# Performance work log

Hardware: AMD Instinct MI355X
Metric: run time of the kernel (lower is better)

The kernel has to match this reference:

```python
import jax, jax.numpy as jnp
import numpy as np

B, C, E, TOPK = 8192, 1024, 8, 4
H = 4 * C  # mlp_ratio = 4.0
EPS = 1e-6


def quick_gelu(x):
    return x * jax.nn.sigmoid(1.702 * x)


def layer_norm(x, gamma, beta):
    mu = jnp.mean(x, axis=-1, keepdims=True)
    var = jnp.var(x, axis=-1, keepdims=True)
    return (x - mu) * jax.lax.rsqrt(var + EPS) * gamma + beta


def setup_inputs() -> dict:
    key = jax.random.key(0)
    ks = jax.random.split(key, 8)
    s1 = 1.0 / np.sqrt(C)
    s2 = 1.0 / np.sqrt(H)
    return {
        "x": jax.random.normal(ks[0], (B, C), dtype=jnp.float32),
        "W1": jax.random.uniform(ks[1], (E, C, H), jnp.float32, -s1, s1),
        "b1": jax.random.uniform(ks[2], (E, H), jnp.float32, -s1, s1),
        "W2": jax.random.uniform(ks[3], (E, H, C), jnp.float32, -s2, s2),
        "b2": jax.random.uniform(ks[4], (E, C), jnp.float32, -s2, s2),
        "ln_g": jnp.ones((E, C), jnp.float32),
        "ln_b": jnp.zeros((E, C), jnp.float32),
        "Wg": jax.random.uniform(ks[5], (C, E), jnp.float32, -s1, s1),
        "bg": jax.random.uniform(ks[6], (E,), jnp.float32, -s1, s1),
    }


def reference(x, W1, b1, W2, b2, ln_g, ln_b, Wg, bg):
    # gate + softmax + top-k
    scores = jax.nn.softmax(x @ Wg + bg, axis=-1)           # [B, E]
    topk_scores, topk_idx = jax.lax.top_k(scores, TOPK)     # [B, K]
    # all experts on all tokens (naive MoE, matches original)
    h = quick_gelu(jnp.einsum('bc,ech->beh', x, W1) + b1)   # [B, E, H]
    y = quick_gelu(jnp.einsum('beh,ehc->bec', h, W2) + b2)  # [B, E, C]
    y = layer_norm(y, ln_g, ln_b)                            # [B, E, C]
    # gather top-k expert outputs and weighted-combine
    topk_out = jnp.take_along_axis(y, topk_idx[:, :, None], axis=1)  # [B, K, C]
    return jnp.sum(topk_out * topk_scores[:, :, None], axis=1)       # [B, C]
```

## Files before the change

### kernel.cpp

```cpp
#include <hip/hip_runtime.h>

#define NB 8192
#define NC 1024
#define NE 8
#define NK 4
#define NH 4096
constexpr int ROWCAP = NB * NK + NE * 128;

typedef _Float16 f16;
typedef _Float16 f16x8 __attribute__((ext_vector_type(8)));
typedef _Float16 f16x4 __attribute__((ext_vector_type(4)));
typedef float    f32x4 __attribute__((ext_vector_type(4)));

__device__ __forceinline__ void async_cp16(const f16* g, f16* l) {
    __builtin_amdgcn_global_load_lds((const __attribute__((address_space(1))) void*)g,
                                     (__attribute__((address_space(3))) void*)l, 16, 0, 0);
}

__device__ __forceinline__ float quick_gelu(float v) {
    return v / (1.f + __expf(-1.702f * v));
}

__global__ void transpose_cast_k(const float* __restrict__ in, f16* __restrict__ out,
                                 int R, int S) {
    __shared__ f16 tile[32][33];
    int e = blockIdx.z;
    long base = (long)e * R * S;
    int s0 = blockIdx.x * 32, r0 = blockIdx.y * 32;
    int tx = threadIdx.x & 31, ty = threadIdx.x >> 5;
    #pragma unroll
    for (int i = 0; i < 32; i += 8)
        tile[ty + i][tx] = (f16)in[base + (long)(r0 + ty + i) * S + s0 + tx];
    __syncthreads();
    #pragma unroll
    for (int i = 0; i < 32; i += 8)
        out[base + (long)(s0 + ty + i) * R + r0 + tx] = tile[tx][ty + i];
}

__global__ void gating_k(const float* __restrict__ x, const float* __restrict__ Wg,
                         const float* __restrict__ bg, int* __restrict__ counts,
                         int* __restrict__ tokmap, int* __restrict__ eids,
                         int* __restrict__ slots, float* __restrict__ gatew,
                         f16* __restrict__ x16) {
    int b = blockIdx.x, t = threadIdx.x;
    float acc[NE] = {};
    float4 xv = ((const float4*)(x + (long)b * NC))[t];
    f16x4 hx = { (f16)xv.x, (f16)xv.y, (f16)xv.z, (f16)xv.w };
    ((f16x4*)(x16 + (long)b * NC))[t] = hx;
    const float* wr = Wg + (long)t * 4 * NE;
    #pragma unroll
    for (int j = 0; j < 4; j++) {
        float xj = ((const float*)&xv)[j];
        #pragma unroll
        for (int e2 = 0; e2 < NE; e2++) acc[e2] += xj * wr[j * NE + e2];
    }
    #pragma unroll
    for (int e2 = 0; e2 < NE; e2++)
        #pragma unroll
        for (int off = 32; off; off >>= 1) acc[e2] += __shfl_down(acc[e2], off);
    __shared__ float red[4][NE];
    int lane = t & 63, w = t >> 6;
    if (lane == 0)
        for (int e2 = 0; e2 < NE; e2++) red[w][e2] = acc[e2];
    __syncthreads();
    if (t == 0) {
        float l[NE];
        float m = -1e30f;
        for (int e2 = 0; e2 < NE; e2++) {
            l[e2] = red[0][e2] + red[1][e2] + red[2][e2] + red[3][e2] + bg[e2];
            m = fmaxf(m, l[e2]);
        }
        float p[NE], sum = 0.f;
        for (int e2 = 0; e2 < NE; e2++) { p[e2] = __expf(l[e2] - m); sum += p[e2]; }
        float inv = 1.f / sum;
        for (int e2 = 0; e2 < NE; e2++) p[e2] *= inv;
        bool taken[NE] = {};
        for (int k = 0; k < NK; k++) {
            int be = 0; float bv = -1e30f;
            for (int e2 = 0; e2 < NE; e2++)
                if (!taken[e2] && p[e2] > bv) { bv = p[e2]; be = e2; }
            taken[be] = true;
            int slot = atomicAdd(&counts[be], 1);
            tokmap[be * NB + slot] = b;
            eids[b * NK + k] = be;
            slots[b * NK + k] = slot;
            gatew[b * NK + k] = bv;
        }
    }
}

__global__ void offsets_k(const int* __restrict__ counts, int* __restrict__ offp) {
    if (threadIdx.x == 0 && blockIdx.x == 0) {
        int o = 0;
        for (int e = 0; e < NE; e++) { offp[e] = o; o += ((counts[e] + 127) >> 7) << 7; }
    }
}

__global__ __launch_bounds__(256) void gemm_f16(
    const f16* __restrict__ A, const f16* __restrict__ Bt,
    const float* __restrict__ bias, f16* __restrict__ Out,
    const int* __restrict__ counts, const int* __restrict__ offp,
    const int* __restrict__ tokmap, int Kd, int N, int gather) {
    int e = blockIdx.z;
    int cnt = counts[e];
    int m0 = blockIdx.x << 7;
    if (m0 >= cnt) return;
    int n0 = blockIdx.y << 7;
    int base = offp[e];

    __shared__ __align__(16) f16 smem[16384];

    int t = threadIdx.x;
    int lane = t & 63;
    int w = t >> 6;
    int wm = (w >> 1) << 6, wn = (w & 1) << 6;

    int sr = m0 + (t >> 2);
    int sc = (((t & 3) ^ ((t >> 3) & 3)) << 3);
    int ca = sr < cnt - 1 ? sr : cnt - 1;
    int cb = sr + 64 < cnt - 1 ? sr + 64 : cnt - 1;
    long arow0, arow1;
    if (gather) { arow0 = tokmap[e * NB + ca]; arow1 = tokmap[e * NB + cb]; }
    else        { arow0 = base + ca;           arow1 = base + cb; }
    const f16* ap0 = A + arow0 * (long)Kd + sc;
    const f16* ap1 = A + arow1 * (long)Kd + sc;
    const f16* bp0 = Bt + ((long)e * N + n0 + (t >> 2)) * (long)Kd + sc;
    const f16* bp1 = bp0 + (long)64 * Kd;

    auto stage = [&](int q) {
        f16* d = smem + (q << 13) + (t << 3);
        async_cp16(ap0, d);        ap0 += 32;
        async_cp16(ap1, d + 2048); ap1 += 32;
        async_cp16(bp0, d + 4096); bp0 += 32;
        async_cp16(bp1, d + 6144); bp1 += 32;
    };

    f32x4 acc[4][4] = {};
    int ml = lane & 15;
    int sxq = (((lane >> 4) ^ ((ml >> 1) & 3)) << 3);
    int aoff = (wm + ml) * 32 + sxq;
    int boff = (wn + ml) * 32 + sxq + 4096;

    int nIter = Kd >> 5;
    stage(0);
    __syncthreads();
    for (int it = 0; it < nIter; ++it) {
        int p = it & 1;
        if (it + 1 < nIter) stage(p ^ 1);
        const f16* sb = smem + (p << 13);
        f16x8 af[4], bf[4];
        #pragma unroll
        for (int mi = 0; mi < 4; mi++) af[mi] = *(const f16x8*)(sb + aoff + mi * 512);
        #pragma unroll
        for (int ni = 0; ni < 4; ni++) bf[ni] = *(const f16x8*)(sb + boff + ni * 512);
        #pragma unroll
        for (int mi = 0; mi < 4; mi++)
            #pragma unroll
            for (int ni = 0; ni < 4; ni++)
                acc[mi][ni] = __builtin_amdgcn_mfma_f32_16x16x32_f16(af[mi], bf[ni], acc[mi][ni], 0, 0, 0);
        __syncthreads();
    }

    const int EP = 136;
    int rq = (lane >> 4) << 2;
    #pragma unroll
    for (int h = 0; h < 2; ++h) {
        if (wm == h * 64) {
            #pragma unroll
            for (int ni = 0; ni < 4; ni++) {
                int col = wn + ni * 16 + ml;
                float bv = bias[(long)e * N + n0 + col];
                #pragma unroll
                for (int mi = 0; mi < 4; mi++) {
                    #pragma unroll
                    for (int rr = 0; rr < 4; rr++) {
                        int lr = mi * 16 + rq + rr;
                        smem[lr * EP + col] = (f16)quick_gelu(acc[mi][ni][rr] + bv);
                    }
                }
            }
        }
        __syncthreads();
        int r = t >> 2;
        int grow = m0 + h * 64 + r;
        if (grow < cnt) {
            long gbase = (long)(base + grow) * N + n0;
            #pragma unroll
            for (int j = 0; j < 4; j++) {
                int cc = ((t & 3) + 4 * j) << 3;
                *(f16x8*)(Out + gbase + cc) = *(const f16x8*)&smem[r * EP + cc];
            }
        }
        __syncthreads();
    }
}

__global__ void ln_combine_k(const f16* __restrict__ y16, const float* __restrict__ lng,
                             const float* __restrict__ lnb, const int* __restrict__ eids,
                             const int* __restrict__ slots, const float* __restrict__ gatew,
                             const int* __restrict__ offp, float* __restrict__ out) {
    int b = blockIdx.x, t = threadIdx.x;
    int lane = t & 63, w = t >> 6;
    __shared__ float red[4][2];
    float o[4] = {0.f, 0.f, 0.f, 0.f};
    int c0 = t * 4;
    for (int k = 0; k < NK; k++) {
        int e = eids[b * NK + k];
        long r = offp[e] + slots[b * NK + k];
        float wk = gatew[b * NK + k];
        f16x4 hv = *(const f16x4*)(y16 + r * NC + c0);
        float v[4];
        #pragma unroll
        for (int j = 0; j < 4; j++) v[j] = (float)hv[j];
        float s = v[0] + v[1] + v[2] + v[3];
        float ss = v[0] * v[0] + v[1] * v[1] + v[2] * v[2] + v[3] * v[3];
        #pragma unroll
        for (int off = 32; off; off >>= 1) { s += __shfl_down(s, off); ss += __shfl_down(ss, off); }
        if (lane == 0) { red[w][0] = s; red[w][1] = ss; }
        __syncthreads();
        float S  = red[0][0] + red[1][0] + red[2][0] + red[3][0];
        float SS = red[0][1] + red[1][1] + red[2][1] + red[3][1];
        float mu = S * (1.f / NC);
        float var = SS * (1.f / NC) - mu * mu;
        float rs = rsqrtf(var + 1e-6f);
        #pragma unroll
        for (int j = 0; j < 4; j++) {
            float g  = lng[(long)e * NC + c0 + j];
            float bb = lnb[(long)e * NC + c0 + j];
            o[j] += wk * ((v[j] - mu) * rs * g + bb);
        }
        __syncthreads();
    }
    float4 ov = {o[0], o[1], o[2], o[3]};
    ((float4*)(out + (long)b * NC))[t] = ov;
}

extern "C" void kernel_launch(void* const* d_in, const int* in_sizes, int n_in,
                              void* d_out, int out_size, void* d_ws, size_t ws_size,
                              hipStream_t stream) {
    const float* x   = (const float*)d_in[0];
    const float* W1  = (const float*)d_in[1];
    const float* b1  = (const float*)d_in[2];
    const float* W2  = (const float*)d_in[3];
    const float* b2  = (const float*)d_in[4];
    const float* lng = (const float*)d_in[5];
    const float* lnb = (const float*)d_in[6];
    const float* Wg  = (const float*)d_in[7];
    const float* bg  = (const float*)d_in[8];
    float* out = (float*)d_out;

    char* ws = (char*)d_ws;
    size_t o = 0;
    auto take = [&](size_t bytes) { char* p = ws + o; o += (bytes + 255) & ~(size_t)255; return p; };
    f16*   x16    = (f16*)take((size_t)NB * NC * 2);
    f16*   w1t    = (f16*)take((size_t)NE * NH * NC * 2);
    f16*   w2t    = (f16*)take((size_t)NE * NC * NH * 2);
    f16*   h16    = (f16*)take((size_t)ROWCAP * NH * 2);
    f16*   y16    = (f16*)take((size_t)ROWCAP * NC * 2);
    int*   tokmap = (int*)take((size_t)NE * NB * 4);
    int*   eids   = (int*)take((size_t)NB * NK * 4);
    int*   slots  = (int*)take((size_t)NB * NK * 4);
    float* gatew  = (float*)take((size_t)NB * NK * 4);
    int*   counts = (int*)take(256);
    int*   offp   = (int*)take(256);

    hipMemsetAsync(counts, 0, NE * sizeof(int), stream);
    transpose_cast_k<<<dim3(NH / 32, NC / 32, NE), 256, 0, stream>>>(W1, w1t, NC, NH);
    transpose_cast_k<<<dim3(NC / 32, NH / 32, NE), 256, 0, stream>>>(W2, w2t, NH, NC);
    gating_k<<<NB, 256, 0, stream>>>(x, Wg, bg, counts, tokmap, eids, slots, gatew, x16);
    offsets_k<<<1, 64, 0, stream>>>(counts, offp);
    gemm_f16<<<dim3(64, NH / 128, NE), 256, 0, stream>>>(x16, w1t, b1, h16, counts, offp, tokmap, NC, NH, 1);
    gemm_f16<<<dim3(64, NC / 128, NE), 256, 0, stream>>>(h16, w2t, b2, y16, counts, offp, tokmap, NH, NC, 0);
    ln_combine_k<<<NB, 256, 0, stream>>>(y16, lng, lnb, eids, slots, gatew, offp, out);
}
```

Measured before the change: 1.859 ms.

## Replace expert GEMM with 256x256 tile, 4-stage async pipeline, split waits

Replaces the 128x128, 256-thread, double-buffered expert GEMM with a 256x256 tile run by 512 threads. It adds a four-slab LDS ring with async global-to-LDS copies three slabs ahead, explicit vmcnt/lgkmcnt waits and barriers, and raised wave priority around the MFMA bursts. Each wave computes its M half in two passes so loads of the next A fragments overlap the current MFMAs. The aim is more reuse per LDS byte and more overlap of loads with compute. The trade-offs are that the XOR swizzle on LDS is dropped, which may cause bank conflicts, the 128 KB LDS footprint limits occupancy, and 256-row tiles waste more work on partially filled expert segments.

```diff
diff --git a/kernel.cpp b/kernel.cpp
--- a/kernel.cpp
+++ b/kernel.cpp
@@ -96,99 +96,130 @@
     }
 }
 
-__global__ __launch_bounds__(256) void gemm_f16(
+__global__ __launch_bounds__(512, 2) void gemm256(
     const f16* __restrict__ A, const f16* __restrict__ Bt,
     const float* __restrict__ bias, f16* __restrict__ Out,
     const int* __restrict__ counts, const int* __restrict__ offp,
     const int* __restrict__ tokmap, int Kd, int N, int gather) {
     int e = blockIdx.z;
     int cnt = counts[e];
-    int m0 = blockIdx.x << 7;
+    int m0 = blockIdx.x << 8;
     if (m0 >= cnt) return;
-    int n0 = blockIdx.y << 7;
+    int n0 = blockIdx.y << 8;
     int base = offp[e];
 
-    __shared__ __align__(16) f16 smem[16384];
+    __shared__ __align__(16) f16 smem[65536];
+    f16* As = smem;
+    f16* Bs = smem + 32768;
 
     int t = threadIdx.x;
     int lane = t & 63;
     int w = t >> 6;
-    int wm = (w >> 1) << 6, wn = (w & 1) << 6;
-
-    int sr = m0 + (t >> 2);
-    int sc = (((t & 3) ^ ((t >> 3) & 3)) << 3);
-    int ca = sr < cnt - 1 ? sr : cnt - 1;
-    int cb = sr + 64 < cnt - 1 ? sr + 64 : cnt - 1;
-    long arow0, arow1;
-    if (gather) { arow0 = tokmap[e * NB + ca]; arow1 = tokmap[e * NB + cb]; }
-    else        { arow0 = base + ca;           arow1 = base + cb; }
+    int wr = w >> 2, wc = w & 3;
+    int ml = lane & 15, kq = lane >> 4;
+
+    int sr = t >> 2;
+    int sc = (t & 3) << 3;
+    int ra = m0 + sr;        if (ra > cnt - 1) ra = cnt - 1;
+    int rb = m0 + sr + 128;  if (rb > cnt - 1) rb = cnt - 1;
+    long arow0 = gather ? (long)tokmap[e * NB + ra] : (long)(base + ra);
+    long arow1 = gather ? (long)tokmap[e * NB + rb] : (long)(base + rb);
     const f16* ap0 = A + arow0 * (long)Kd + sc;
     const f16* ap1 = A + arow1 * (long)Kd + sc;
-    const f16* bp0 = Bt + ((long)e * N + n0 + (t >> 2)) * (long)Kd + sc;
-    const f16* bp1 = bp0 + (long)64 * Kd;
-
-    auto stage = [&](int q) {
-        f16* d = smem + (q << 13) + (t << 3);
-        async_cp16(ap0, d);        ap0 += 32;
-        async_cp16(ap1, d + 2048); ap1 += 32;
-        async_cp16(bp0, d + 4096); bp0 += 32;
-        async_cp16(bp1, d + 6144); bp1 += 32;
+    const f16* bp0 = Bt + ((long)e * N + n0 + sr) * (long)Kd + sc;
+    const f16* bp1 = bp0 + (long)128 * Kd;
+    f16* adst = As + t * 8;
+    f16* bdst = Bs + t * 8;
+
+    auto stageA = [&](int slab) {
+        f16* d = adst + ((slab & 3) << 13);
+        int ko = slab << 5;
+        async_cp16(ap0 + ko, d);
+        async_cp16(ap1 + ko, d + 4096);
     };
-
-    f32x4 acc[4][4] = {};
-    int ml = lane & 15;
-    int sxq = (((lane >> 4) ^ ((ml >> 1) & 3)) << 3);
-    int aoff = (wm + ml) * 32 + sxq;
-    int boff = (wn + ml) * 32 + sxq + 4096;
-
-    int nIter = Kd >> 5;
-    stage(0);
-    __syncthreads();
-    for (int it = 0; it < nIter; ++it) {
-        int p = it & 1;
-        if (it + 1 < nIter) stage(p ^ 1);
-        const f16* sb = smem + (p << 13);
+    auto stageB = [&](int slab) {
+        f16* d = bdst + ((slab & 3) << 13);
+        int ko = slab << 5;
+        async_cp16(bp0 + ko, d);
+        async_cp16(bp1 + ko, d + 4096);
+    };
+
+    int aoff = (wr * 128 + ml) * 32 + kq * 8;
+    int boff = (wc * 64 + ml) * 32 + kq * 8;
+
+    f32x4 acc[8][4] = {};
+
+    int NSl = Kd >> 5;
+
+    stageA(0); stageB(0); stageA(1); stageB(1); stageA(2); stageB(2);
+    asm volatile("s_waitcnt vmcnt(8)" ::: "memory");
+    __builtin_amdgcn_s_barrier();
+
+    for (int s = 0; s < NSl; ++s) {
+        const f16* as = As + ((s & 3) << 13);
+        const f16* bs = Bs + ((s & 3) << 13);
         f16x8 af[4], bf[4];
         #pragma unroll
-        for (int mi = 0; mi < 4; mi++) af[mi] = *(const f16x8*)(sb + aoff + mi * 512);
-        #pragma unroll
-        for (int ni = 0; ni < 4; ni++) bf[ni] = *(const f16x8*)(sb + boff + ni * 512);
-        #pragma unroll
-        for (int mi = 0; mi < 4; mi++)
+        for (int mi = 0; mi < 4; ++mi) af[mi] = *(const f16x8*)(as + aoff + mi * 512);
+        #pragma unroll
+        for (int ni = 0; ni < 4; ++ni) bf[ni] = *(const f16x8*)(bs + boff + ni * 512);
+        if (s + 3 < NSl) stageA(s + 3);
+        __builtin_amdgcn_s_barrier();
+        asm volatile("s_waitcnt lgkmcnt(0)" ::: "memory");
+        __builtin_amdgcn_s_setprio(1);
+        #pragma unroll
+        for (int mi = 0; mi < 4; ++mi)
             #pragma unroll
-            for (int ni = 0; ni < 4; ni++)
+            for (int ni = 0; ni < 4; ++ni)
                 acc[mi][ni] = __builtin_amdgcn_mfma_f32_16x16x32_f16(af[mi], bf[ni], acc[mi][ni], 0, 0, 0);
-        __syncthreads();
-    }
-
-    const int EP = 136;
-    int rq = (lane >> 4) << 2;
+        __builtin_amdgcn_s_setprio(0);
+        __builtin_amdgcn_s_barrier();
+        f16x8 ag[4];
+        #pragma unroll
+        for (int mi = 0; mi < 4; ++mi) ag[mi] = *(const f16x8*)(as + aoff + (4 + mi) * 512);
+        if (s + 3 < NSl) stageB(s + 3);
+        if (s <= NSl - 4)      asm volatile("s_waitcnt vmcnt(8)" ::: "memory");
+        else if (s == NSl - 3) asm volatile("s_waitcnt vmcnt(4)" ::: "memory");
+        else if (s == NSl - 2) asm volatile("s_waitcnt vmcnt(0)" ::: "memory");
+        __builtin_amdgcn_s_barrier();
+        asm volatile("s_waitcnt lgkmcnt(0)" ::: "memory");
+        __builtin_amdgcn_s_setprio(1);
+        #pragma unroll
+        for (int mi = 0; mi < 4; ++mi)
+            #pragma unroll
+            for (int ni = 0; ni < 4; ++ni)
+                acc[4 + mi][ni] = __builtin_amdgcn_mfma_f32_16x16x32_f16(ag[mi], bf[ni], acc[4 + mi][ni], 0, 0, 0);
+        __builtin_amdgcn_s_setprio(0);
+        __builtin_amdgcn_s_barrier();
+    }
+
+    const int EP = 272;
+    int r = t >> 2;
     #pragma unroll
     for (int h = 0; h < 2; ++h) {
-        if (wm == h * 64) {
+        if (wr == h) {
             #pragma unroll
-            for (int ni = 0; ni < 4; ni++) {
-                int col = wn + ni * 16 + ml;
+            for (int ni = 0; ni < 4; ++ni) {
+                int col = wc * 64 + ni * 16 + ml;
                 float bv = bias[(long)e * N + n0 + col];
                 #pragma unroll
-                for (int mi = 0; mi < 4; mi++) {
+                for (int mi = 0; mi < 8; ++mi) {
                     #pragma unroll
-                    for (int rr = 0; rr < 4; rr++) {
-                        int lr = mi * 16 + rq + rr;
+                    for (int rr = 0; rr < 4; ++rr) {
+                        int lr = mi * 16 + kq * 4 + rr;
                         smem[lr * EP + col] = (f16)quick_gelu(acc[mi][ni][rr] + bv);
                     }
                 }
             }
         }
         __syncthreads();
-        int r = t >> 2;
-        int grow = m0 + h * 64 + r;
+        int grow = m0 + h * 128 + r;
         if (grow < cnt) {
-            long gbase = (long)(base + grow) * N + n0;
+            long gb = (long)(base + grow) * N + n0;
             #pragma unroll
-            for (int j = 0; j < 4; j++) {
+            for (int j = 0; j < 8; ++j) {
                 int cc = ((t & 3) + 4 * j) << 3;
-                *(f16x8*)(Out + gbase + cc) = *(const f16x8*)&smem[r * EP + cc];
+                *(f16x8*)(Out + gb + cc) = *(const f16x8*)&smem[r * EP + cc];
             }
         }
         __syncthreads();
@@ -269,7 +300,7 @@
     transpose_cast_k<<<dim3(NC / 32, NH / 32, NE), 256, 0, stream>>>(W2, w2t, NH, NC);
     gating_k<<<NB, 256, 0, stream>>>(x, Wg, bg, counts, tokmap, eids, slots, gatew, x16);
     offsets_k<<<1, 64, 0, stream>>>(counts, offp);
-    gemm_f16<<<dim3(64, NH / 128, NE), 256, 0, stream>>>(x16, w1t, b1, h16, counts, offp, tokmap, NC, NH, 1);
-    gemm_f16<<<dim3(64, NC / 128, NE), 256, 0, stream>>>(h16, w2t, b2, y16, counts, offp, tokmap, NH, NC, 0);
+    gemm256<<<dim3(NB / 256, NH / 256, NE), 512, 0, stream>>>(x16, w1t, b1, h16, counts, offp, tokmap, NC, NH, 1);
+    gemm256<<<dim3(NB / 256, NC / 256, NE), 512, 0, stream>>>(h16, w2t, b2, y16, counts, offp, tokmap, NH, NC, 0);
     ln_combine_k<<<NB, 256, 0, stream>>>(y16, lng, lnb, eids, slots, gatew, offp, out);
 }
```

New measurement: 1.939 ms. 4.3% more time.

## Triple-buffer GEMM K-slabs with partial vmcnt waits and MFMA priority

Applied to the files above, without the earlier changes.

Moves the GEMM main loop from double to triple buffering of 32-wide K slabs in LDS, with loads issued two slabs ahead. The full __syncthreads is replaced by a partial s_waitcnt vmcnt that only waits for the oldest slab, plus a raw barrier, so global loads stay in flight across iterations. The MFMA block is wrapped in s_setprio to favour the math wave. This raises LDS use to 48KB per block, which may lower occupancy.

```diff
diff --git a/kernel.cpp b/kernel.cpp
--- a/kernel.cpp
+++ b/kernel.cpp
@@ -108,7 +108,7 @@
     int n0 = blockIdx.y << 7;
     int base = offp[e];
 
-    __shared__ __align__(16) f16 smem[16384];
+    __shared__ __align__(16) f16 smem[24576];
 
     int t = threadIdx.x;
     int lane = t & 63;
@@ -127,12 +127,13 @@
     const f16* bp0 = Bt + ((long)e * N + n0 + (t >> 2)) * (long)Kd + sc;
     const f16* bp1 = bp0 + (long)64 * Kd;
 
-    auto stage = [&](int q) {
-        f16* d = smem + (q << 13) + (t << 3);
-        async_cp16(ap0, d);        ap0 += 32;
-        async_cp16(ap1, d + 2048); ap1 += 32;
-        async_cp16(bp0, d + 4096); bp0 += 32;
-        async_cp16(bp1, d + 6144); bp1 += 32;
+    auto stage = [&](int slab, int slot) {
+        f16* d = smem + slot * 8192 + (t << 3);
+        int ko = slab << 5;
+        async_cp16(ap0 + ko, d);
+        async_cp16(ap1 + ko, d + 2048);
+        async_cp16(bp0 + ko, d + 4096);
+        async_cp16(bp1 + ko, d + 6144);
     };
 
     f32x4 acc[4][4] = {};
@@ -141,24 +142,36 @@
     int aoff = (wm + ml) * 32 + sxq;
     int boff = (wn + ml) * 32 + sxq + 4096;
 
-    int nIter = Kd >> 5;
-    stage(0);
-    __syncthreads();
-    for (int it = 0; it < nIter; ++it) {
-        int p = it & 1;
-        if (it + 1 < nIter) stage(p ^ 1);
-        const f16* sb = smem + (p << 13);
+    int NSl = Kd >> 5;
+
+    stage(0, 0); stage(1, 1);
+    asm volatile("s_waitcnt vmcnt(4)" ::: "memory");
+    __builtin_amdgcn_s_barrier();
+    asm volatile("" ::: "memory");
+
+    int sl = 0, sl2 = 2;
+    for (int it = 0; it < NSl; ++it) {
+        if (it + 2 < NSl) stage(it + 2, sl2);
+        const f16* sb = smem + sl * 8192;
         f16x8 af[4], bf[4];
         #pragma unroll
         for (int mi = 0; mi < 4; mi++) af[mi] = *(const f16x8*)(sb + aoff + mi * 512);
         #pragma unroll
         for (int ni = 0; ni < 4; ni++) bf[ni] = *(const f16x8*)(sb + boff + ni * 512);
+        asm volatile("s_waitcnt lgkmcnt(0)" ::: "memory");
+        __builtin_amdgcn_s_setprio(1);
         #pragma unroll
         for (int mi = 0; mi < 4; mi++)
             #pragma unroll
             for (int ni = 0; ni < 4; ni++)
                 acc[mi][ni] = __builtin_amdgcn_mfma_f32_16x16x32_f16(af[mi], bf[ni], acc[mi][ni], 0, 0, 0);
-        __syncthreads();
+        __builtin_amdgcn_s_setprio(0);
+        if (it < NSl - 2)       asm volatile("s_waitcnt vmcnt(4)" ::: "memory");
+        else if (it == NSl - 2) asm volatile("s_waitcnt vmcnt(0)" ::: "memory");
+        __builtin_amdgcn_s_barrier();
+        asm volatile("" ::: "memory");
+        sl  = (sl  == 2) ? 0 : sl  + 1;
+        sl2 = (sl2 == 2) ? 0 : sl2 + 1;
     }
 
     const int EP = 136;
```

After: 1.733 ms. 6.7% less time.
